# Kernel optimization log

Measured on AMD Instinct MI355X. Metric: run time of the kernel, lower is better.

## Reference

```python
import jax, jax.numpy as jnp
import numpy as np

B, S, D = 2, 2048, 1024
H = 16
HD = D // H  # 64
ROPE_BASE = 10000.0


def rotate_half(x):
    x1, x2 = jnp.split(x, 2, axis=-1)
    return jnp.concatenate((-x2, x1), axis=-1)


def rope_cos_sin(seq_len, dim, dtype):
    inv_freq = 1.0 / (ROPE_BASE ** (jnp.arange(0, dim, 2, dtype=jnp.float32) / dim))
    t = jnp.arange(seq_len, dtype=jnp.float32)
    freqs = jnp.einsum('i,j->ij', t, inv_freq)          # [S, dim/2]
    emb = jnp.concatenate((freqs, freqs), axis=-1)      # [S, dim]
    return jnp.cos(emb).astype(dtype), jnp.sin(emb).astype(dtype)


def setup_inputs() -> dict:
    key = jax.random.key(0)
    ks = jax.random.split(key, 5)
    std = 0.02
    return {
        'x': jax.random.normal(ks[0], (B, S, D), dtype=jnp.float32),
        'wq': jax.random.normal(ks[1], (D, D), dtype=jnp.float32) * std,
        'wk': jax.random.normal(ks[2], (D, D), dtype=jnp.float32) * std,
        'wv': jax.random.normal(ks[3], (D, D), dtype=jnp.float32) * std,
        'wo': jax.random.normal(ks[4], (D, D), dtype=jnp.float32) * std,
    }


def reference(x, wq, wk, wv, wo):
    b, s, d = x.shape
    # Q/K/V projections (nn.Linear: x @ W.T)
    q = jnp.einsum('bsd,ed->bse', x, wq).reshape(b, s, H, HD).transpose(0, 2, 1, 3)
    k = jnp.einsum('bsd,ed->bse', x, wk).reshape(b, s, H, HD).transpose(0, 2, 1, 3)
    v = jnp.einsum('bsd,ed->bse', x, wv).reshape(b, s, H, HD).transpose(0, 2, 1, 3)
    # RoPE
    cos, sin = rope_cos_sin(s, HD, x.dtype)  # [s, HD]
    cos = cos[None, None]  # [1,1,s,HD]
    sin = sin[None, None]
    q = q * cos + rotate_half(q) * sin
    k = k * cos + rotate_half(k) * sin
    # Causal SDPA
    scale = HD ** -0.5
    scores = jnp.einsum('bhqd,bhkd->bhqk', q, k) * scale
    causal = jnp.tril(jnp.ones((s, s), dtype=bool))
    scores = jnp.where(causal[None, None], scores, jnp.finfo(scores.dtype).min)
    attn = jax.nn.softmax(scores, axis=-1)
    out = jnp.einsum('bhqk,bhkd->bhqd', attn, v)
    out = out.transpose(0, 2, 1, 3).reshape(b, s, d)
    return jnp.einsum('bsd,ed->bse', out, wo)
```

## Files before the change

kernel.cpp:

```cpp
#include <hip/hip_runtime.h>
#include <hip/hip_bf16.h>
#include <cstdint>
#include <cstddef>

#define BDIM 2
#define SDIM 2048
#define DDIM 1024
#define HN   16
#define HDIM 64

using bf16 = __bf16;
typedef __attribute__((ext_vector_type(8))) __bf16 bf16x8;
typedef __attribute__((ext_vector_type(4))) __bf16 bf16x4;
typedef __attribute__((ext_vector_type(8))) unsigned short ushort8;
typedef __attribute__((ext_vector_type(4))) float  f32x4;

#define MFMA16(a, b, c) __builtin_amdgcn_mfma_f32_16x16x32_bf16((a), (b), (c), 0, 0, 0)

#define ASYNC16(g, l)                                                          \
  __builtin_amdgcn_global_load_lds(                                            \
      (const __attribute__((address_space(1))) void*)(g),                      \
      (__attribute__((address_space(3))) void*)(l), 16, 0, 0)

#define QSCALE 0.1803368801111204f

__global__ __launch_bounds__(256) void cvt_bf16(const float* __restrict__ src,
                                                bf16* __restrict__ dst, int n4) {
  int i = blockIdx.x * 256 + threadIdx.x;
  if (i < n4) {
    float4 v = ((const float4*)src)[i];
    bf16x4 o = {(__bf16)v.x, (__bf16)v.y, (__bf16)v.z, (__bf16)v.w};
    *(bf16x4*)(dst + (size_t)i * 4) = o;
  }
}

struct Ptr4 { const float* p[4]; };
__global__ __launch_bounds__(256) void cvt_w(Ptr4 srcs, bf16* __restrict__ dst) {
  const int seg = blockIdx.y;
  const float* src = srcs.p[seg];
  int i = blockIdx.x * 256 + threadIdx.x;
  float4 v = ((const float4*)src)[i];
  bf16x4 o = {(__bf16)v.x, (__bf16)v.y, (__bf16)v.z, (__bf16)v.w};
  *(bf16x4*)(dst + (size_t)seg * (DDIM * DDIM) + (size_t)i * 4) = o;
}

__global__ __launch_bounds__(256) void rope_table(float* __restrict__ cosT,
                                                  float* __restrict__ sinT) {
  int i = blockIdx.x * 256 + threadIdx.x;
  int s = i >> 5, j = i & 31;
  float inv = powf(10000.f, -(float)j * (1.f / 32.f));
  float a = (float)s * inv;
  float sn, c;
  sincosf(a, &sn, &c);
  cosT[s * 64 + j]      = c;
  cosT[s * 64 + j + 32] = c;
  sinT[s * 64 + j]      = sn;
  sinT[s * 64 + j + 32] = sn;
}

__global__ __launch_bounds__(256) void fixup_qkv(bf16* __restrict__ q,
                                                 bf16* __restrict__ k,
                                                 const unsigned short* __restrict__ v,
                                                 unsigned short* __restrict__ vt,
                                                 const float* __restrict__ cosT,
                                                 const float* __restrict__ sinT) {
  const int bh = blockIdx.y;
  const int s0 = blockIdx.x * 32;
  const int tid = threadIdx.x;

  {
    const int s = s0 + (tid >> 3);
    const int j0 = (tid & 7) * 4;
    const size_t base = ((size_t)bh * SDIM + s) * HDIM;
    const float4 c4 = *(const float4*)(cosT + s * 64 + j0);
    const float4 s4 = *(const float4*)(sinT + s * 64 + j0);
    const float cc[4] = {c4.x, c4.y, c4.z, c4.w};
    const float ss[4] = {s4.x, s4.y, s4.z, s4.w};

    bf16x4 qlo = *(bf16x4*)(q + base + j0);
    bf16x4 qhi = *(bf16x4*)(q + base + j0 + 32);
    bf16x4 klo = *(bf16x4*)(k + base + j0);
    bf16x4 khi = *(bf16x4*)(k + base + j0 + 32);
    bf16x4 rql, rqh, rkl, rkh;
#pragma unroll
    for (int e = 0; e < 4; ++e) {
      float a = (float)qlo[e], b = (float)qhi[e];
      rql[e] = (__bf16)((a * cc[e] - b * ss[e]) * QSCALE);
      rqh[e] = (__bf16)((b * cc[e] + a * ss[e]) * QSCALE);
      a = (float)klo[e]; b = (float)khi[e];
      rkl[e] = (__bf16)(a * cc[e] - b * ss[e]);
      rkh[e] = (__bf16)(b * cc[e] + a * ss[e]);
    }
    *(bf16x4*)(q + base + j0)      = rql;
    *(bf16x4*)(q + base + j0 + 32) = rqh;
    *(bf16x4*)(k + base + j0)      = rkl;
    *(bf16x4*)(k + base + j0 + 32) = rkh;
  }

  {
    const int w = tid >> 6, d = tid & 63;
    const int sb = s0 + w * 8;
    const unsigned short* src = v + ((size_t)bh * SDIM + sb) * HDIM + d;
    ushort8 o;
#pragma unroll
    for (int j = 0; j < 8; ++j) o[j] = src[(size_t)j * HDIM];
    *(ushort8*)(vt + ((size_t)bh * HDIM + d) * SDIM + sb) = o;
  }
}

template <int MODE>
__global__ __launch_bounds__(256) void gemm_bt(const bf16* __restrict__ A,
                                               const bf16* __restrict__ B0,
                                               void* __restrict__ C0) {
  constexpr int K = 1024;
  __shared__ __align__(16) bf16 As[128 * 64];
  __shared__ __align__(16) bf16 Bs[128 * 64];
  const int tid = threadIdx.x;
  const int l = tid & 63, w = tid >> 6;
  const int wr = w >> 1, wc = w & 1;
  const int lr = l & 15, lg = l >> 4;
  const int bm = blockIdx.y * 128;
  const int bn = blockIdx.x * 128;
  const bf16* Bw = B0 + (size_t)blockIdx.z * (1024 * 1024);

  f32x4 acc[4][4] = {};

  for (int k0 = 0; k0 < K; k0 += 64) {
    __syncthreads();
#pragma unroll
    for (int i = 0; i < 4; ++i) {
      int idx = i * 2048 + tid * 8;
      int row = idx >> 6, col = idx & 63;
      ASYNC16(A + (size_t)(bm + row) * K + (k0 + col), As + idx);
      ASYNC16(Bw + (size_t)(bn + row) * K + (k0 + col), Bs + idx);
    }
    __syncthreads();
#pragma unroll
    for (int c = 0; c < 2; ++c) {
      bf16x8 af[4], bfr[4];
#pragma unroll
      for (int m = 0; m < 4; ++m)
        af[m] = *(const bf16x8*)(As + (wr * 64 + m * 16 + lr) * 64 + c * 32 + lg * 8);
#pragma unroll
      for (int n = 0; n < 4; ++n)
        bfr[n] = *(const bf16x8*)(Bs + (wc * 64 + n * 16 + lr) * 64 + c * 32 + lg * 8);
      __builtin_amdgcn_s_setprio(1);
#pragma unroll
      for (int m = 0; m < 4; ++m)
#pragma unroll
        for (int n = 0; n < 4; ++n)
          acc[m][n] = MFMA16(af[m], bfr[n], acc[m][n]);
      __builtin_amdgcn_s_setprio(0);
    }
  }

#pragma unroll
  for (int m = 0; m < 4; ++m) {
#pragma unroll
    for (int n = 0; n < 4; ++n) {
#pragma unroll
      for (int r = 0; r < 4; ++r) {
        int row = bm + wr * 64 + m * 16 + lg * 4 + r;
        int col = bn + wc * 64 + n * 16 + lr;
        float v = acc[m][n][r];
        if constexpr (MODE == 0) {
          bf16* C = (bf16*)C0 + (size_t)blockIdx.z * ((size_t)BDIM * SDIM * DDIM);
          size_t off = (((size_t)(row >> 11) * HN + (col >> 6)) * SDIM + (row & (SDIM - 1))) * HDIM + (col & 63);
          C[off] = (__bf16)v;
        } else {
          ((float*)C0)[(size_t)row * DDIM + col] = v;
        }
      }
    }
  }
}

__global__ __launch_bounds__(512) void attn_fwd(const bf16* __restrict__ qg,
                                                const bf16* __restrict__ kg,
                                                const bf16* __restrict__ vtg,
                                                bf16* __restrict__ og) {
  __shared__ __align__(16) bf16 Sl[2][3][4096];
  __shared__ __align__(16) bf16 Pl[8][1024];

  const int tid = threadIdx.x;
  const int l = tid & 63, w = tid >> 6;
  const int g = w >> 2, wg = w & 3;
  const int lr = l & 15, lg = l >> 4;
  const int bh = blockIdx.x;
  const int qt = 31 - blockIdx.y;
  const int q0 = qt * 64;
  const size_t hb = (size_t)bh * SDIM * HDIM;
  const bf16* Q  = qg + hb;
  const bf16* Kp = kg + hb;
  const bf16* Vp = vtg + hb;
  const int b = bh >> 4, h = bh & 15;
  bf16* Pw = &Pl[w][0];
  const int swz = lr & 7;

  const int mm0 = 2 * wg, mm1 = 2 * wg + 1;
  const int f0 = mm0 & 3, c0 = mm0 >> 2;
  const int f1 = mm1 & 3, c1 = mm1 >> 2;
  const int lo0 = mm0 * 512 + l * 8;
  const int lo1 = mm1 * 512 + l * 8;
  bf16* const SlG = &Sl[g][0][0];

  bf16x8 qf[2];
#pragma unroll
  for (int c = 0; c < 2; ++c)
    qf[c] = *(const bf16x8*)(Q + (size_t)(q0 + wg * 16 + lr) * HDIM + c * 32 + lg * 8);

  f32x4 o[4] = {};
  float m = -3e38f, lsum = 0.f;

  const int ng   = (qt >= g) ? ((qt - g) >> 1) + 1 : 0;
  const int smax = (qt >> 1) + 1;

  const bf16* kN0 = Kp + (size_t)(f0 * 16 + lr) * HDIM + c0 * 32 + lg * 8 + (size_t)g * 64 * HDIM;
  const bf16* kN1 = Kp + (size_t)(f1 * 16 + lr) * HDIM + c1 * 32 + lg * 8 + (size_t)g * 64 * HDIM;
  const bf16* vN0 = Vp + (size_t)(f0 * 16 + lr) * SDIM + c0 * 32 + lg * 8 + g * 64;
  const bf16* vN1 = Vp + (size_t)(f1 * 16 + lr) * SDIM + c1 * 32 + lg * 8 + g * 64;

  if (ng > 0) {
    ASYNC16(kN0, SlG + 0 * 4096 + lo0); kN0 += 128 * HDIM;
    ASYNC16(kN1, SlG + 0 * 4096 + lo1); kN1 += 128 * HDIM;
    ASYNC16(vN0, SlG + 1 * 4096 + lo0); vN0 += 128;
    ASYNC16(vN1, SlG + 1 * 4096 + lo1); vN1 += 128;
  }
  __syncthreads();

  int ks = 0, vs = 1;
  for (int s = 0; s < smax; ++s) {
    const int t = 2 * s + g;
    const bool act = (s < ng);
    const int kn = 3 - ks - vs;
    const bool hasNext = act && (s + 1 < ng);

    if (hasNext) {
      ASYNC16(kN0, SlG + kn * 4096 + lo0); kN0 += 128 * HDIM;
      ASYNC16(kN1, SlG + kn * 4096 + lo1); kN1 += 128 * HDIM;
    }

    const bool diag = (t == qt);
    const int fLim = diag ? wg : 3;

    f32x4 sc[4] = {};
    if (act) {
      __builtin_amdgcn_s_setprio(1);
#pragma unroll
      for (int c = 0; c < 2; ++c)
#pragma unroll
        for (int f = 0; f < 4; ++f)
          if (f <= fLim) {
            bf16x8 kfr = *(const bf16x8*)(SlG + ks * 4096 + (c * 4 + f) * 512 + l * 8);
            sc[f] = MFMA16(kfr, qf[c], sc[f]);
          }
      __builtin_amdgcn_s_setprio(0);
    }

    __builtin_amdgcn_s_barrier();
    __builtin_amdgcn_sched_barrier(0);

    if (hasNext) {
      ASYNC16(vN0, SlG + ks * 4096 + lo0); vN0 += 128;
      ASYNC16(vN1, SlG + ks * 4096 + lo1); vN1 += 128;
    }

    if (act) {
      if (diag) {
#pragma unroll
        for (int f = 0; f < 4; ++f)
#pragma unroll
          for (int r = 0; r < 4; ++r) {
            if (f > wg)
              sc[f][r] = -3e38f;
            else if (f == wg)
              sc[f][r] = (lg * 4 + r <= lr) ? sc[f][r] : -3e38f;
          }
      }

      float mxl = -3e38f;
#pragma unroll
      for (int f = 0; f < 4; ++f)
#pragma unroll
        for (int r = 0; r < 4; ++r) mxl = fmaxf(mxl, sc[f][r]);

      if (!__all(mxl - m <= 8.f)) {
        float mx = fmaxf(mxl, __shfl_xor(mxl, 16));
        mx = fmaxf(mx, __shfl_xor(mx, 32));
        float mnew = fmaxf(m, mx);
        float corr = exp2f(m - mnew);
        m = mnew;
        lsum *= corr;
        float cb[4];
#pragma unroll
        for (int r = 0; r < 4; ++r) cb[r] = __shfl(corr, lg * 4 + r);
#pragma unroll
        for (int n = 0; n < 4; ++n)
#pragma unroll
          for (int r = 0; r < 4; ++r) o[n][r] *= cb[r];
      }

      float rs = 0.f;
#pragma unroll
      for (int f = 0; f < 4; ++f) {
        float p0 = exp2f(sc[f][0] - m);
        float p1 = exp2f(sc[f][1] - m);
        float p2 = exp2f(sc[f][2] - m);
        float p3 = exp2f(sc[f][3] - m);
        rs += (p0 + p1) + (p2 + p3);
        bf16x4 pv = {(__bf16)p0, (__bf16)p1, (__bf16)p2, (__bf16)p3};
        const int ch = f * 2 + (lg >> 1);
        *(bf16x4*)(Pw + lr * 64 + ((ch ^ swz) << 3) + (lg & 1) * 4) = pv;
      }
      lsum += rs;

      const int cLim = diag ? (wg >> 1) : 1;
      __builtin_amdgcn_s_setprio(1);
#pragma unroll
      for (int c = 0; c < 2; ++c)
        if (c <= cLim) {
          bf16x8 pf = *(const bf16x8*)(Pw + lr * 64 + (((c * 4 + lg) ^ swz) << 3));
#pragma unroll
          for (int n = 0; n < 4; ++n) {
            bf16x8 vfr = *(const bf16x8*)(SlG + vs * 4096 + (c * 4 + n) * 512 + l * 8);
            o[n] = MFMA16(pf, vfr, o[n]);
          }
        }
      __builtin_amdgcn_s_setprio(0);
    }

    __syncthreads();
    vs = ks;
    ks = kn;
  }

  float* Osh = (float*)&Sl[0][0][0];
  float* Msh = Osh + 4096;
  float* Lsh = Msh + 256;

  if (g == 1) {
    Msh[wg * 64 + l] = m;
    Lsh[wg * 64 + l] = lsum;
#pragma unroll
    for (int n = 0; n < 4; ++n)
#pragma unroll
      for (int r = 0; r < 4; ++r)
        Osh[((wg * 4 + n) * 4 + r) * 64 + l] = o[n][r];
  }
  __syncthreads();

  if (g == 0) {
    float m1 = Msh[wg * 64 + l], l1 = Lsh[wg * 64 + l];
    float mt = fmaxf(m, m1);
    float a0 = exp2f(m - mt), a1 = exp2f(m1 - mt);
    float lt = lsum * a0 + l1 * a1;
    lt += __shfl_xor(lt, 16);
    lt += __shfl_xor(lt, 32);
    float a0b[4], a1b[4], ltb[4];
#pragma unroll
    for (int r = 0; r < 4; ++r) {
      a0b[r] = __shfl(a0, lg * 4 + r);
      a1b[r] = __shfl(a1, lg * 4 + r);
      ltb[r] = __shfl(lt, lg * 4 + r);
    }
#pragma unroll
    for (int r = 0; r < 4; ++r) {
      float rl = 1.f / ltb[r];
      int qr = q0 + 16 * wg + lg * 4 + r;
#pragma unroll
      for (int n = 0; n < 4; ++n) {
        float o1 = Osh[((wg * 4 + n) * 4 + r) * 64 + l];
        og[((size_t)(b * SDIM + qr)) * DDIM + h * HDIM + n * 16 + lr] =
            (__bf16)((o[n][r] * a0b[r] + o1 * a1b[r]) * rl);
      }
    }
  }
}

extern "C" void kernel_launch(void* const* d_in, const int* in_sizes, int n_in,
                              void* d_out, int out_size, void* d_ws, size_t ws_size,
                              hipStream_t stream) {
  const float* x  = (const float*)d_in[0];
  const float* wq = (const float*)d_in[1];
  const float* wk = (const float*)d_in[2];
  const float* wv = (const float*)d_in[3];
  const float* wo = (const float*)d_in[4];

  char* ws = (char*)d_ws;
  const size_t MB = 1024 * 1024;
  bf16* xb   = (bf16*)(ws + 0);
  bf16* wqb  = (bf16*)(ws + 8 * MB);
  bf16* wob  = (bf16*)(ws + 14 * MB);
  bf16* qb   = (bf16*)(ws + 16 * MB);
  bf16* kb   = (bf16*)(ws + 24 * MB);
  bf16* vb   = (bf16*)(ws + 32 * MB);
  bf16* ob   = (bf16*)(ws + 40 * MB);
  float* cosT = (float*)(ws + 48 * MB);
  float* sinT = (float*)(ws + 49 * MB);
  bf16* vtb  = xb;

  const int NX = BDIM * SDIM * DDIM;
  const int NW = DDIM * DDIM;

  cvt_bf16<<<NX / 4 / 256, 256, 0, stream>>>(x, xb, NX / 4);
  Ptr4 wsrc{{wq, wk, wv, wo}};
  cvt_w<<<dim3(NW / 4 / 256, 4), 256, 0, stream>>>(wsrc, wqb);
  rope_table<<<(SDIM * 32) / 256, 256, 0, stream>>>(cosT, sinT);
  gemm_bt<0><<<dim3(8, 32, 3), 256, 0, stream>>>(xb, wqb, (void*)qb);
  fixup_qkv<<<dim3(SDIM / 32, 32), 256, 0, stream>>>(qb, kb, (const unsigned short*)vb,
                                                     (unsigned short*)vtb, cosT, sinT);
  attn_fwd<<<dim3(32, 32), 512, 0, stream>>>(qb, kb, vtb, ob);
  gemm_bt<1><<<dim3(8, 32, 1), 256, 0, stream>>>(ob, wob, d_out);
}
```

Before: 136.0 us.

## Rewrite QKV projection as double-buffered 256x256 GEMM writing transposed V directly

Replaces the 128x128 single-buffered QKV GEMM with a 512-thread kernel using 256x256 tiles, double-buffered async LDS loads and a swizzled block order. The V slice is stored already transposed from the epilogue, so the separate V transpose pass in the fixup kernel is dropped and the fixup now only applies RoPE to Q and K. The aim is more data reuse and load/compute overlap in the projection plus less memory traffic. The trade-offs are 128KB of LDS per block, only 192 blocks, and strided 8-byte stores into Vt.

Measured after the change: 146.9 us. 8.0% more time.

```diff
diff --git a/kernel.cpp b/kernel.cpp
--- a/kernel.cpp
+++ b/kernel.cpp
@@ -12,7 +12,6 @@
 using bf16 = __bf16;
 typedef __attribute__((ext_vector_type(8))) __bf16 bf16x8;
 typedef __attribute__((ext_vector_type(4))) __bf16 bf16x4;
-typedef __attribute__((ext_vector_type(8))) unsigned short ushort8;
 typedef __attribute__((ext_vector_type(4))) float  f32x4;
 
 #define MFMA16(a, b, c) __builtin_amdgcn_mfma_f32_16x16x32_bf16((a), (b), (c), 0, 0, 0)
@@ -58,60 +57,145 @@
   sinT[s * 64 + j + 32] = sn;
 }
 
-__global__ __launch_bounds__(256) void fixup_qkv(bf16* __restrict__ q,
-                                                 bf16* __restrict__ k,
-                                                 const unsigned short* __restrict__ v,
-                                                 unsigned short* __restrict__ vt,
-                                                 const float* __restrict__ cosT,
-                                                 const float* __restrict__ sinT) {
+__global__ __launch_bounds__(256) void fixup_qk(bf16* __restrict__ q,
+                                                bf16* __restrict__ k,
+                                                const float* __restrict__ cosT,
+                                                const float* __restrict__ sinT) {
   const int bh = blockIdx.y;
-  const int s0 = blockIdx.x * 32;
+  const int s = blockIdx.x * 32 + (threadIdx.x >> 3);
+  const int j0 = (threadIdx.x & 7) * 4;
+  const size_t base = ((size_t)bh * SDIM + s) * HDIM;
+  const float4 c4 = *(const float4*)(cosT + s * 64 + j0);
+  const float4 s4 = *(const float4*)(sinT + s * 64 + j0);
+  const float cc[4] = {c4.x, c4.y, c4.z, c4.w};
+  const float ss[4] = {s4.x, s4.y, s4.z, s4.w};
+
+  bf16x4 qlo = *(bf16x4*)(q + base + j0);
+  bf16x4 qhi = *(bf16x4*)(q + base + j0 + 32);
+  bf16x4 klo = *(bf16x4*)(k + base + j0);
+  bf16x4 khi = *(bf16x4*)(k + base + j0 + 32);
+  bf16x4 rql, rqh, rkl, rkh;
+#pragma unroll
+  for (int e = 0; e < 4; ++e) {
+    float a = (float)qlo[e], b = (float)qhi[e];
+    rql[e] = (__bf16)((a * cc[e] - b * ss[e]) * QSCALE);
+    rqh[e] = (__bf16)((b * cc[e] + a * ss[e]) * QSCALE);
+    a = (float)klo[e]; b = (float)khi[e];
+    rkl[e] = (__bf16)(a * cc[e] - b * ss[e]);
+    rkh[e] = (__bf16)(b * cc[e] + a * ss[e]);
+  }
+  *(bf16x4*)(q + base + j0)      = rql;
+  *(bf16x4*)(q + base + j0 + 32) = rqh;
+  *(bf16x4*)(k + base + j0)      = rkl;
+  *(bf16x4*)(k + base + j0 + 32) = rkh;
+}
+
+__global__ __launch_bounds__(512) void gemm_qkv(const bf16* __restrict__ A,
+                                                const bf16* __restrict__ Bw,
+                                                bf16* __restrict__ C0,
+                                                bf16* __restrict__ Vt) {
+  constexpr int K = 1024;
+  __shared__ __align__(16) bf16 As[2][256 * 64];
+  __shared__ __align__(16) bf16 Bs[2][256 * 64];
   const int tid = threadIdx.x;
-
-  {
-    const int s = s0 + (tid >> 3);
-    const int j0 = (tid & 7) * 4;
-    const size_t base = ((size_t)bh * SDIM + s) * HDIM;
-    const float4 c4 = *(const float4*)(cosT + s * 64 + j0);
-    const float4 s4 = *(const float4*)(sinT + s * 64 + j0);
-    const float cc[4] = {c4.x, c4.y, c4.z, c4.w};
-    const float ss[4] = {s4.x, s4.y, s4.z, s4.w};
-
-    bf16x4 qlo = *(bf16x4*)(q + base + j0);
-    bf16x4 qhi = *(bf16x4*)(q + base + j0 + 32);
-    bf16x4 klo = *(bf16x4*)(k + base + j0);
-    bf16x4 khi = *(bf16x4*)(k + base + j0 + 32);
-    bf16x4 rql, rqh, rkl, rkh;
-#pragma unroll
-    for (int e = 0; e < 4; ++e) {
-      float a = (float)qlo[e], b = (float)qhi[e];
-      rql[e] = (__bf16)((a * cc[e] - b * ss[e]) * QSCALE);
-      rqh[e] = (__bf16)((b * cc[e] + a * ss[e]) * QSCALE);
-      a = (float)klo[e]; b = (float)khi[e];
-      rkl[e] = (__bf16)(a * cc[e] - b * ss[e]);
-      rkh[e] = (__bf16)(b * cc[e] + a * ss[e]);
-    }
-    *(bf16x4*)(q + base + j0)      = rql;
-    *(bf16x4*)(q + base + j0 + 32) = rqh;
-    *(bf16x4*)(k + base + j0)      = rkl;
-    *(bf16x4*)(k + base + j0 + 32) = rkh;
-  }
-
-  {
-    const int w = tid >> 6, d = tid & 63;
-    const int sb = s0 + w * 8;
-    const unsigned short* src = v + ((size_t)bh * SDIM + sb) * HDIM + d;
-    ushort8 o;
-#pragma unroll
-    for (int j = 0; j < 8; ++j) o[j] = src[(size_t)j * HDIM];
-    *(ushort8*)(vt + ((size_t)bh * HDIM + d) * SDIM + sb) = o;
-  }
-}
-
-template <int MODE>
-__global__ __launch_bounds__(256) void gemm_bt(const bf16* __restrict__ A,
-                                               const bf16* __restrict__ B0,
-                                               void* __restrict__ C0) {
+  const int l = tid & 63, w = tid >> 6;
+  const int wr = w >> 2, wc = w & 3;
+  const int lr = l & 15, lg = l >> 4;
+
+  const int bid = blockIdx.x;
+  const int swb = (bid & 7) * 24 + (bid >> 3);
+  const int mt = swb & 15, nt = swb >> 4;
+  const int bm = mt * 256, bn = nt * 256;
+
+  f32x4 acc[8][4] = {};
+
+  auto stage = [&](int buf, int k0) {
+#pragma unroll
+    for (int i = 0; i < 4; ++i) {
+      int lin = i * 4096 + tid * 8;
+      int row = lin >> 6, col = lin & 63;
+      ASYNC16(A + (size_t)(bm + row) * K + (k0 + col), As[buf] + lin);
+      ASYNC16(Bw + (size_t)(bn + row) * K + (k0 + col), Bs[buf] + lin);
+    }
+  };
+
+  stage(0, 0);
+  asm volatile("s_waitcnt vmcnt(0)" ::: "memory");
+  __builtin_amdgcn_s_barrier();
+
+  for (int k = 0; k < 16; ++k) {
+    const int cur = k & 1;
+    if (k < 15) {
+      stage(cur ^ 1, (k + 1) * 64);
+      asm volatile("s_waitcnt vmcnt(8)" ::: "memory");
+    } else {
+      asm volatile("s_waitcnt vmcnt(0)" ::: "memory");
+    }
+    __builtin_amdgcn_sched_barrier(0);
+    __builtin_amdgcn_s_barrier();
+
+    const bf16* Ab = As[cur];
+    const bf16* Bb = Bs[cur];
+#pragma unroll
+    for (int kc = 0; kc < 2; ++kc) {
+      bf16x8 a[8], b[4];
+#pragma unroll
+      for (int m = 0; m < 8; ++m)
+        a[m] = *(const bf16x8*)(Ab + (wr * 128 + m * 16 + lr) * 64 + kc * 32 + lg * 8);
+#pragma unroll
+      for (int n = 0; n < 4; ++n)
+        b[n] = *(const bf16x8*)(Bb + (wc * 64 + n * 16 + lr) * 64 + kc * 32 + lg * 8);
+      __builtin_amdgcn_s_setprio(1);
+#pragma unroll
+      for (int m = 0; m < 8; ++m)
+#pragma unroll
+        for (int n = 0; n < 4; ++n)
+          acc[m][n] = MFMA16(a[m], b[n], acc[m][n]);
+      __builtin_amdgcn_s_setprio(0);
+    }
+    __builtin_amdgcn_sched_barrier(0);
+    __builtin_amdgcn_s_barrier();
+    __builtin_amdgcn_sched_barrier(0);
+  }
+
+  const int z = bn >> 10;
+  const int bcol = bn & 1023;
+  if (z < 2) {
+    bf16* C = C0 + (size_t)z * ((size_t)BDIM * SDIM * DDIM);
+#pragma unroll
+    for (int m = 0; m < 8; ++m) {
+      const int row0 = bm + wr * 128 + m * 16 + lg * 4;
+      const int bb = row0 >> 11, s = row0 & (SDIM - 1);
+#pragma unroll
+      for (int n = 0; n < 4; ++n) {
+        const int h = (bcol >> 6) + wc;
+        const int hd = n * 16 + lr;
+        const size_t base = ((size_t)(bb * HN + h) * SDIM + s) * HDIM + hd;
+#pragma unroll
+        for (int r = 0; r < 4; ++r)
+          C[base + (size_t)r * HDIM] = (__bf16)acc[m][n][r];
+      }
+    }
+  } else {
+#pragma unroll
+    for (int m = 0; m < 8; ++m) {
+      const int row0 = bm + wr * 128 + m * 16 + lg * 4;
+      const int bb = row0 >> 11, s0 = row0 & (SDIM - 1);
+#pragma unroll
+      for (int n = 0; n < 4; ++n) {
+        const int h = (bcol >> 6) + wc;
+        const int hd = n * 16 + lr;
+        bf16x4 pv = {(__bf16)acc[m][n][0], (__bf16)acc[m][n][1],
+                     (__bf16)acc[m][n][2], (__bf16)acc[m][n][3]};
+        *(bf16x4*)(Vt + ((size_t)(bb * HN + h) * HDIM + hd) * SDIM + s0) = pv;
+      }
+    }
+  }
+}
+
+__global__ __launch_bounds__(256) void gemm_out(const bf16* __restrict__ A,
+                                                const bf16* __restrict__ Bw,
+                                                float* __restrict__ C) {
   constexpr int K = 1024;
   __shared__ __align__(16) bf16 As[128 * 64];
   __shared__ __align__(16) bf16 Bs[128 * 64];
@@ -121,7 +205,6 @@
   const int lr = l & 15, lg = l >> 4;
   const int bm = blockIdx.y * 128;
   const int bn = blockIdx.x * 128;
-  const bf16* Bw = B0 + (size_t)blockIdx.z * (1024 * 1024);
 
   f32x4 acc[4][4] = {};
 
@@ -155,24 +238,15 @@
   }
 
 #pragma unroll
-  for (int m = 0; m < 4; ++m) {
-#pragma unroll
-    for (int n = 0; n < 4; ++n) {
+  for (int m = 0; m < 4; ++m)
+#pragma unroll
+    for (int n = 0; n < 4; ++n)
 #pragma unroll
       for (int r = 0; r < 4; ++r) {
         int row = bm + wr * 64 + m * 16 + lg * 4 + r;
         int col = bn + wc * 64 + n * 16 + lr;
-        float v = acc[m][n][r];
-        if constexpr (MODE == 0) {
-          bf16* C = (bf16*)C0 + (size_t)blockIdx.z * ((size_t)BDIM * SDIM * DDIM);
-          size_t off = (((size_t)(row >> 11) * HN + (col >> 6)) * SDIM + (row & (SDIM - 1))) * HDIM + (col & 63);
-          C[off] = (__bf16)v;
-        } else {
-          ((float*)C0)[(size_t)row * DDIM + col] = v;
-        }
-      }
-    }
-  }
+        C[(size_t)row * DDIM + col] = acc[m][n][r];
+      }
 }
 
 __global__ __launch_bounds__(512) void attn_fwd(const bf16* __restrict__ qg,
@@ -393,11 +467,10 @@
   bf16* wob  = (bf16*)(ws + 14 * MB);
   bf16* qb   = (bf16*)(ws + 16 * MB);
   bf16* kb   = (bf16*)(ws + 24 * MB);
-  bf16* vb   = (bf16*)(ws + 32 * MB);
+  bf16* vtb  = (bf16*)(ws + 32 * MB);
   bf16* ob   = (bf16*)(ws + 40 * MB);
   float* cosT = (float*)(ws + 48 * MB);
   float* sinT = (float*)(ws + 49 * MB);
-  bf16* vtb  = xb;
 
   const int NX = BDIM * SDIM * DDIM;
   const int NW = DDIM * DDIM;
@@ -406,9 +479,8 @@
   Ptr4 wsrc{{wq, wk, wv, wo}};
   cvt_w<<<dim3(NW / 4 / 256, 4), 256, 0, stream>>>(wsrc, wqb);
   rope_table<<<(SDIM * 32) / 256, 256, 0, stream>>>(cosT, sinT);
-  gemm_bt<0><<<dim3(8, 32, 3), 256, 0, stream>>>(xb, wqb, (void*)qb);
-  fixup_qkv<<<dim3(SDIM / 32, 32), 256, 0, stream>>>(qb, kb, (const unsigned short*)vb,
-                                                     (unsigned short*)vtb, cosT, sinT);
+  gemm_qkv<<<192, 512, 0, stream>>>(xb, wqb, qb, vtb);
+  fixup_qk<<<dim3(SDIM / 32, 32), 256, 0, stream>>>(qb, kb, cosT, sinT);
   attn_fwd<<<dim3(32, 32), 512, 0, stream>>>(qb, kb, vtb, ob);
-  gemm_bt<1><<<dim3(8, 32, 1), 256, 0, stream>>>(ob, wob, d_out);
-}
+  gemm_out<<<dim3(8, 32), 256, 0, stream>>>(ob, wob, (float*)d_out);
+}
```
